# Optimization experiments

Measured on AMD Instinct MI355X. Metric: run time of the kernel, lower is better.

## Reference

```python
import jax, jax.numpy as jnp
import numpy as np

H = 16          # num_attention_heads
D = 1024        # hidden_size
HD = D // H     # attention_head_size = 64


def setup_inputs() -> dict:
    key = jax.random.key(0)
    ks = jax.random.split(key, 9)
    s = 1.0 / np.sqrt(D)
    return {
        "hidden_states": jax.random.normal(ks[0], (4, 1024, D), jnp.float32),
        "encoder_hidden_states": jax.random.normal(ks[1], (4, 1024, D), jnp.float32),
        "attention_mask": jnp.zeros((4, 1, 1, 2048), jnp.float32),
        "Wq": jax.random.normal(ks[2], (D, D), jnp.float32) * s,
        "bq": jnp.zeros((D,), jnp.float32),
        "Wk": jax.random.normal(ks[3], (D, D), jnp.float32) * s,
        "bk": jnp.zeros((D,), jnp.float32),
        "Wv": jax.random.normal(ks[4], (D, D), jnp.float32) * s,
        "bv": jnp.zeros((D,), jnp.float32),
    }


def _split_heads(x):
    # [B, S, D] -> [B, H, S, HD]
    B, S, _ = x.shape
    return x.reshape(B, S, H, HD).transpose(0, 2, 1, 3)


def reference(hidden_states, encoder_hidden_states, attention_mask, Wq, bq, Wk, bk, Wv, bv):
    # KV over concat(encoder, decoder); Q over decoder hidden states only.
    all_hidden = jnp.concatenate([encoder_hidden_states, hidden_states], axis=1)  # [B, Skv, D]
    q = _split_heads(hidden_states @ Wq + bq)        # [B, H, Sq, HD]
    k = _split_heads(all_hidden @ Wk + bk)           # [B, H, Skv, HD]
    v = _split_heads(all_hidden @ Wv + bv)           # [B, H, Skv, HD]

    scores = jnp.einsum("bhqd,bhkd->bhqk", q, k) / np.sqrt(HD).astype(np.float32)
    scores = scores + attention_mask                 # additive mask, broadcast
    probs = jax.nn.softmax(scores, axis=-1)          # dropout p=0 (eval)
    ctx = jnp.einsum("bhqk,bhkd->bhqd", probs, v)    # [B, H, Sq, HD]
    B, _, Sq, _ = ctx.shape
    return ctx.transpose(0, 2, 1, 3).reshape(B, Sq, D)
```

## Files before the change

### kernel.cpp

```cpp
#include <hip/hip_runtime.h>


typedef _Float16 f16;
typedef __attribute__((ext_vector_type(4))) _Float16 half4;
typedef __attribute__((ext_vector_type(8))) _Float16 half8;
typedef __attribute__((ext_vector_type(4))) float floatx4;
typedef __attribute__((ext_vector_type(16))) float floatx16;
typedef __attribute__((ext_vector_type(4))) unsigned int uint4v;

__global__ void wt_kernel(const float* __restrict__ W, f16* __restrict__ Wt) {
    __shared__ float tile[32][33];
    int k0 = blockIdx.y * 32, n0 = blockIdx.x * 32;
    int tx = threadIdx.x, ty = threadIdx.y;
    #pragma unroll
    for (int i = 0; i < 32; i += 8)
        tile[ty + i][tx] = W[(k0 + ty + i) * 1024 + n0 + tx];
    __syncthreads();
    #pragma unroll
    for (int i = 0; i < 32; i += 8)
        Wt[(n0 + ty + i) * 1024 + k0 + tx] = (f16)tile[tx][ty + i];
}

__global__ void cvt_kernel(const float* __restrict__ hid, const float* __restrict__ enc,
                           f16* __restrict__ Aall) {
    int t = blockIdx.x * 256 + threadIdx.x;
    int rowg = t >> 7, col = (t & 127) * 8;
    int b = rowg >> 11, r = rowg & 2047;
    const float* src = (r < 1024 ? enc + ((size_t)b * 1024 + r) * 1024
                                 : hid + ((size_t)b * 1024 + (r - 1024)) * 1024) + col;
    float4 v0 = *(const float4*)src, v1 = *(const float4*)(src + 4);
    half8 o;
    o[0] = (f16)v0.x; o[1] = (f16)v0.y; o[2] = (f16)v0.z; o[3] = (f16)v0.w;
    o[4] = (f16)v1.x; o[5] = (f16)v1.y; o[6] = (f16)v1.z; o[7] = (f16)v1.w;
    *(half8*)(Aall + (size_t)rowg * 1024 + col) = o;
}

__launch_bounds__(256)
__global__ void qkv_gemm(const f16* __restrict__ Aall, const f16* __restrict__ Wt,
                         const float* __restrict__ bias, f16* __restrict__ out, int mode) {
    __shared__ f16 At[128 * 40];
    __shared__ f16 Bt[128 * 40];

    int tid = threadIdx.x;
    int m0 = blockIdx.x * 128, n0 = blockIdx.y * 128;
    int wid = tid >> 6, lane = tid & 63;
    int wm = (wid >> 1) * 64, wn = (wid & 1) * 64;
    int lr = lane & 15, lg = lane >> 4;

    floatx4 acc[4][4];
    #pragma unroll
    for (int i = 0; i < 4; i++)
        #pragma unroll
        for (int j = 0; j < 4; j++) acc[i][j] = (floatx4)(0.f);

    int tr2 = tid >> 2, tk2 = (tid & 3) * 8;
    const f16 *a0src, *a1src;
    {
        int mA0 = m0 + tr2, mA1 = mA0 + 64;
        if (mode == 0) {
            int b0 = mA0 >> 10, b1 = mA1 >> 10;
            a0src = Aall + ((size_t)(b0 * 2048 + 1024 + (mA0 & 1023))) * 1024 + tk2;
            a1src = Aall + ((size_t)(b1 * 2048 + 1024 + (mA1 & 1023))) * 1024 + tk2;
        } else {
            a0src = Aall + (size_t)mA0 * 1024 + tk2;
            a1src = Aall + (size_t)mA1 * 1024 + tk2;
        }
    }
    const f16* b0src = Wt + (size_t)(n0 + tr2) * 1024 + tk2;
    const f16* b1src = Wt + (size_t)(n0 + tr2 + 64) * 1024 + tk2;

    half8 ra0 = *(const half8*)a0src, ra1 = *(const half8*)a1src;
    half8 rb0 = *(const half8*)b0src, rb1 = *(const half8*)b1src;

    for (int k0 = 0; k0 < 1024; k0 += 32) {
        __syncthreads();
        *(half8*)&At[tr2 * 40 + tk2]        = ra0;
        *(half8*)&At[(tr2 + 64) * 40 + tk2] = ra1;
        *(half8*)&Bt[tr2 * 40 + tk2]        = rb0;
        *(half8*)&Bt[(tr2 + 64) * 40 + tk2] = rb1;
        __syncthreads();
        if (k0 < 992) {
            ra0 = *(const half8*)(a0src + k0 + 32);
            ra1 = *(const half8*)(a1src + k0 + 32);
            rb0 = *(const half8*)(b0src + k0 + 32);
            rb1 = *(const half8*)(b1src + k0 + 32);
        }

        half8 a[4], bf[4];
        #pragma unroll
        for (int i = 0; i < 4; i++)
            a[i] = *(const half8*)&At[(wm + i * 16 + lr) * 40 + lg * 8];
        #pragma unroll
        for (int j = 0; j < 4; j++)
            bf[j] = *(const half8*)&Bt[(wn + j * 16 + lr) * 40 + lg * 8];
        __builtin_amdgcn_s_setprio(1);
        #pragma unroll
        for (int i = 0; i < 4; i++)
            #pragma unroll
            for (int j = 0; j < 4; j++)
                acc[i][j] = __builtin_amdgcn_mfma_f32_16x16x32_f16(a[i], bf[j], acc[i][j], 0, 0, 0);
        __builtin_amdgcn_s_setprio(0);
    }

    if (mode == 2) {
        #pragma unroll
        for (int i = 0; i < 4; i++) {
            int mbase = m0 + wm + i * 16 + lg * 4;
            int b = mbase >> 11, s = mbase & 2047;
            #pragma unroll
            for (int j = 0; j < 4; j++) {
                int n = n0 + wn + j * 16 + lr;
                int h = n >> 6, d = n & 63;
                float bv = bias[n];
                half4 w;
                #pragma unroll
                for (int r = 0; r < 4; r++) w[r] = (f16)(acc[i][j][r] + bv);
                *(half4*)(out + ((size_t)((b * 16 + h) * 64 + d)) * 2048 + s) = w;
            }
        }
    } else {
        int Sout = (mode == 0) ? 1024 : 2048;
        #pragma unroll
        for (int i = 0; i < 4; i++) {
            int mbase = m0 + wm + i * 16 + lg * 4;
            #pragma unroll
            for (int j = 0; j < 4; j++) {
                int n = n0 + wn + j * 16 + lr;
                int h = n >> 6, d = n & 63;
                float bv = bias[n];
                #pragma unroll
                for (int r = 0; r < 4; r++) {
                    int m = mbase + r;
                    int b = (mode == 0) ? (m >> 10) : (m >> 11);
                    int s = (mode == 0) ? (m & 1023) : (m & 2047);
                    out[((size_t)(b * 16 + h) * Sout + s) * 64 + d] = (f16)(acc[i][j][r] + bv);
                }
            }
        }
    }
}

__device__ inline half8 pack_swap(float s0, float s1, float s2, float s3,
                                  float s4, float s5, float s6, float s7) {
    unsigned a0 = __builtin_bit_cast(unsigned, __builtin_amdgcn_cvt_pkrtz(s0, s1));
    unsigned b0 = __builtin_bit_cast(unsigned, __builtin_amdgcn_cvt_pkrtz(s4, s5));
    unsigned a1 = __builtin_bit_cast(unsigned, __builtin_amdgcn_cvt_pkrtz(s2, s3));
    unsigned b1 = __builtin_bit_cast(unsigned, __builtin_amdgcn_cvt_pkrtz(s6, s7));
    asm("v_permlane32_swap_b32 %0, %1" : "+v"(a0), "+v"(b0));
    asm("v_permlane32_swap_b32 %0, %1" : "+v"(a1), "+v"(b1));
    uint4v w = {a0, a1, b0, b1};
    return __builtin_bit_cast(half8, w);
}

__device__ inline half8 pack_noswap(float s0, float s1, float s2, float s3,
                                    float s4, float s5, float s6, float s7) {
    unsigned w0 = __builtin_bit_cast(unsigned, __builtin_amdgcn_cvt_pkrtz(s0, s1));
    unsigned w1 = __builtin_bit_cast(unsigned, __builtin_amdgcn_cvt_pkrtz(s2, s3));
    unsigned w2 = __builtin_bit_cast(unsigned, __builtin_amdgcn_cvt_pkrtz(s4, s5));
    unsigned w3 = __builtin_bit_cast(unsigned, __builtin_amdgcn_cvt_pkrtz(s6, s7));
    uint4v w = {w0, w1, w2, w3};
    return __builtin_bit_cast(half8, w);
}

__launch_bounds__(256)
__global__ void attn_kernel(const f16* __restrict__ Q, const f16* __restrict__ K,
                            const f16* __restrict__ Vt, const float* __restrict__ mask,
                            float* __restrict__ out) {
    __shared__ f16 Kt[64 * 72];
    __shared__ f16 Vtt[64 * 72];
    __shared__ float maskLds[2048];

    const float LOG2E = 1.4426950408889634f;
    int tid = threadIdx.x;
    int wid = tid >> 6, lane = tid & 63;
    int l31 = lane & 31, l5 = lane >> 5;
    int bh = blockIdx.y, b = bh >> 4, h = bh & 15;
    int q = blockIdx.x * 128 + wid * 32 + l31;

    half8 pa, pcode;
    #pragma unroll
    for (int j = 0; j < 8; j++) { pa[j] = (f16)0; pcode[j] = (f16)(8 * l5 + j); }
    if (l31 < 16 && (l31 >> 3) == l5) pa[l31 & 7] = (f16)1;
    floatx16 pd = __builtin_amdgcn_mfma_f32_32x32x16_f16(pa, pcode, (floatx16)0.f, 0, 0, 0);
    float r4 = __shfl(pd[0], 32);
    bool twoblk = (r4 > 6.0f);

    const float* maskp = mask + b * 2048;
    for (int i = tid; i < 512; i += 256) {
        float4 mv = ((const float4*)maskp)[i];
        mv.x *= LOG2E; mv.y *= LOG2E; mv.z *= LOG2E; mv.w *= LOG2E;
        ((float4*)maskLds)[i] = mv;
    }

    const f16* qrow = Q + ((size_t)bh * 1024 + q) * 64;
    half8 qf[4];
    if (!twoblk) {
        #pragma unroll
        for (int ks = 0; ks < 4; ks++)
            qf[ks] = *(const half8*)(qrow + ks * 16 + l5 * 8);
    } else {
        #pragma unroll
        for (int ks = 0; ks < 4; ks++) {
            half4 lo = *(const half4*)(qrow + ks * 16 + 4 * l5);
            half4 hi = *(const half4*)(qrow + ks * 16 + 8 + 4 * l5);
            qf[ks][0] = lo[0]; qf[ks][1] = lo[1]; qf[ks][2] = lo[2]; qf[ks][3] = lo[3];
            qf[ks][4] = hi[0]; qf[ks][5] = hi[1]; qf[ks][6] = hi[2]; qf[ks][7] = hi[3];
        }
    }
    const f16 qs = (f16)(0.125f * 1.4426950408889634f);
    #pragma unroll
    for (int ks = 0; ks < 4; ks++)
        #pragma unroll
        for (int x = 0; x < 8; x++) qf[ks][x] *= qs;

    floatx16 o0 = (floatx16)0.f, o1 = (floatx16)0.f;
    float m_run = -1e30f, l_run = 0.f;

    int sr = tid >> 2, sc = (tid & 3) * 16;
    const f16* Ksrc = K + ((size_t)bh * 2048 + sr) * 64 + sc;
    const f16* Vsrc = Vt + ((size_t)(bh * 64 + sr)) * 2048 + sc;

    half8 rk0 = *(const half8*)(Ksrc);
    half8 rk1 = *(const half8*)(Ksrc + 8);
    half8 rv0 = *(const half8*)(Vsrc);
    half8 rv1 = *(const half8*)(Vsrc + 8);

    for (int kv0 = 0; kv0 < 2048; kv0 += 64) {
        __syncthreads();
        *(half8*)&Kt[sr * 72 + sc]      = rk0;
        *(half8*)&Kt[sr * 72 + sc + 8]  = rk1;
        *(half8*)&Vtt[sr * 72 + sc]     = rv0;
        *(half8*)&Vtt[sr * 72 + sc + 8] = rv1;
        __syncthreads();
        if (kv0 < 2048 - 64) {
            rk0 = *(const half8*)(Ksrc + (size_t)(kv0 + 64) * 64);
            rk1 = *(const half8*)(Ksrc + (size_t)(kv0 + 64) * 64 + 8);
            rv0 = *(const half8*)(Vsrc + kv0 + 64);
            rv1 = *(const half8*)(Vsrc + kv0 + 64 + 8);
        }

        floatx16 sf0, sf1;
        #pragma unroll
        for (int g = 0; g < 4; g++) {
            float4 mk0 = *(const float4*)&maskLds[kv0 + 8 * g + 4 * l5];
            float4 mk1 = *(const float4*)&maskLds[kv0 + 32 + 8 * g + 4 * l5];
            #pragma unroll
            for (int i = 0; i < 4; i++) {
                sf0[4 * g + i] = ((const float*)&mk0)[i];
                sf1[4 * g + i] = ((const float*)&mk1)[i];
            }
        }

        __builtin_amdgcn_s_setprio(1);
        #pragma unroll
        for (int ks = 0; ks < 4; ks++) {
            half8 k0 = *(const half8*)&Kt[l31 * 72 + ks * 16 + l5 * 8];
            half8 k1 = *(const half8*)&Kt[(32 + l31) * 72 + ks * 16 + l5 * 8];
            sf0 = __builtin_amdgcn_mfma_f32_32x32x16_f16(k0, qf[ks], sf0, 0, 0, 0);
            sf1 = __builtin_amdgcn_mfma_f32_32x32x16_f16(k1, qf[ks], sf1, 0, 0, 0);
        }
        __builtin_amdgcn_s_setprio(0);

        float pmax = -1e30f;
        #pragma unroll
        for (int r = 0; r < 16; r++)
            pmax = fmaxf(pmax, fmaxf(sf0[r], sf1[r]));

        if (!__all(pmax - m_run <= 8.0f)) {
            float rmax = fmaxf(pmax, __shfl_xor(pmax, 32));
            float mnew = fmaxf(m_run, rmax);
            float alpha = exp2f(m_run - mnew);
            l_run *= alpha;
            #pragma unroll
            for (int r = 0; r < 16; r++) { o0[r] *= alpha; o1[r] *= alpha; }
            m_run = mnew;
        }

        float ls = 0.f;
        #pragma unroll
        for (int r = 0; r < 16; r++) {
            float p0 = exp2f(sf0[r] - m_run);
            float p1 = exp2f(sf1[r] - m_run);
            sf0[r] = p0; sf1[r] = p1;
            ls += p0 + p1;
        }
        ls += __shfl_xor(ls, 32);
        l_run += ls;

        half8 pb[4];
        if (!twoblk) {
            pb[0] = pack_swap(sf0[0], sf0[1], sf0[2], sf0[3], sf0[4], sf0[5], sf0[6], sf0[7]);
            pb[1] = pack_swap(sf0[8], sf0[9], sf0[10], sf0[11], sf0[12], sf0[13], sf0[14], sf0[15]);
            pb[2] = pack_swap(sf1[0], sf1[1], sf1[2], sf1[3], sf1[4], sf1[5], sf1[6], sf1[7]);
            pb[3] = pack_swap(sf1[8], sf1[9], sf1[10], sf1[11], sf1[12], sf1[13], sf1[14], sf1[15]);
        } else {
            pb[0] = pack_noswap(sf0[0], sf0[1], sf0[2], sf0[3], sf0[4], sf0[5], sf0[6], sf0[7]);
            pb[1] = pack_noswap(sf0[8], sf0[9], sf0[10], sf0[11], sf0[12], sf0[13], sf0[14], sf0[15]);
            pb[2] = pack_noswap(sf1[0], sf1[1], sf1[2], sf1[3], sf1[4], sf1[5], sf1[6], sf1[7]);
            pb[3] = pack_noswap(sf1[8], sf1[9], sf1[10], sf1[11], sf1[12], sf1[13], sf1[14], sf1[15]);
        }

        __builtin_amdgcn_s_setprio(1);
        #pragma unroll
        for (int kb = 0; kb < 4; kb++) {
            half8 v0 = *(const half8*)&Vtt[l31 * 72 + kb * 16 + l5 * 8];
            half8 v1 = *(const half8*)&Vtt[(32 + l31) * 72 + kb * 16 + l5 * 8];
            o0 = __builtin_amdgcn_mfma_f32_32x32x16_f16(v0, pb[kb], o0, 0, 0, 0);
            o1 = __builtin_amdgcn_mfma_f32_32x32x16_f16(v1, pb[kb], o1, 0, 0, 0);
        }
        __builtin_amdgcn_s_setprio(0);
    }

    float inv = 1.f / l_run;
    float* orow = out + ((size_t)(b * 1024 + q)) * 1024 + h * 64;
    #pragma unroll
    for (int g = 0; g < 4; g++) {
        float4 r0 = {o0[4 * g] * inv, o0[4 * g + 1] * inv, o0[4 * g + 2] * inv, o0[4 * g + 3] * inv};
        float4 r1 = {o1[4 * g] * inv, o1[4 * g + 1] * inv, o1[4 * g + 2] * inv, o1[4 * g + 3] * inv};
        *(float4*)&orow[8 * g + 4 * l5]      = r0;
        *(float4*)&orow[32 + 8 * g + 4 * l5] = r1;
    }
}

extern "C" void kernel_launch(void* const* d_in, const int* in_sizes, int n_in,
                              void* d_out, int out_size, void* d_ws, size_t ws_size,
                              hipStream_t stream) {
    const float* hid  = (const float*)d_in[0];
    const float* enc  = (const float*)d_in[1];
    const float* mask = (const float*)d_in[2];
    const float* Wq   = (const float*)d_in[3];
    const float* bq   = (const float*)d_in[4];
    const float* Wk   = (const float*)d_in[5];
    const float* bk   = (const float*)d_in[6];
    const float* Wv   = (const float*)d_in[7];
    const float* bv   = (const float*)d_in[8];
    float* out = (float*)d_out;

    char* ws = (char*)d_ws;
    f16* Wtq  = (f16*)(ws + ((size_t)0 << 20));
    f16* Wtk  = (f16*)(ws + ((size_t)2 << 20));
    f16* Wtv  = (f16*)(ws + ((size_t)4 << 20));
    f16* Aall = (f16*)(ws + ((size_t)6 << 20));
    f16* Qw   = (f16*)(ws + ((size_t)22 << 20));
    f16* Kw   = (f16*)(ws + ((size_t)30 << 20));
    f16* Vtw  = (f16*)(ws + ((size_t)46 << 20));

    dim3 tb(32, 8);
    wt_kernel<<<dim3(32, 32), tb, 0, stream>>>(Wq, Wtq);
    wt_kernel<<<dim3(32, 32), tb, 0, stream>>>(Wk, Wtk);
    wt_kernel<<<dim3(32, 32), tb, 0, stream>>>(Wv, Wtv);
    cvt_kernel<<<4096, 256, 0, stream>>>(hid, enc, Aall);

    qkv_gemm<<<dim3(32, 8), 256, 0, stream>>>(Aall, Wtq, bq, Qw, 0);
    qkv_gemm<<<dim3(64, 8), 256, 0, stream>>>(Aall, Wtk, bk, Kw, 1);
    qkv_gemm<<<dim3(64, 8), 256, 0, stream>>>(Aall, Wtv, bv, Vtw, 2);

    attn_kernel<<<dim3(8, 64), 256, 0, stream>>>(Qw, Kw, Vtw, mask, out);
}
```

Measured before the change: 168.9 us.

## Use direct global-to-LDS loads in GEMM, prescale mask, remap attention blocks per XCD

The QKV GEMM now loads tiles with global_load_lds straight into unpadded LDS instead of staging them through registers, which drops the register-level prefetch. The three weight-transpose launches are merged into one grid. The mask is prescaled by log2e in a separate small kernel and read from global memory inside the attention loop rather than from LDS. Attention blocks are remapped so that each XCD works on a contiguous set of heads for L2 locality, and the running max starts at 8 instead of -inf. The unpadded LDS layout may cause bank conflicts, and dropping the prefetch exposes global-load latency in the GEMM.

New measurement: 174.4 us. +3.3%, slower.

```diff
diff --git a/kernel.cpp b/kernel.cpp
--- a/kernel.cpp
+++ b/kernel.cpp
@@ -8,8 +8,17 @@
 typedef __attribute__((ext_vector_type(16))) float floatx16;
 typedef __attribute__((ext_vector_type(4))) unsigned int uint4v;
 
-__global__ void wt_kernel(const float* __restrict__ W, f16* __restrict__ Wt) {
+#define GLOAD16(gp, lp)                                                        \
+    __builtin_amdgcn_global_load_lds(                                          \
+        (const __attribute__((address_space(1))) void*)(gp),                   \
+        (__attribute__((address_space(3))) void*)(lp), 16, 0, 0)
+
+__global__ void wt_kernel(const float* __restrict__ Wq, const float* __restrict__ Wk,
+                          const float* __restrict__ Wv, f16* __restrict__ Wtq,
+                          f16* __restrict__ Wtk, f16* __restrict__ Wtv) {
     __shared__ float tile[32][33];
+    const float* W = (blockIdx.z == 0) ? Wq : (blockIdx.z == 1) ? Wk : Wv;
+    f16* Wt = (blockIdx.z == 0) ? Wtq : (blockIdx.z == 1) ? Wtk : Wtv;
     int k0 = blockIdx.y * 32, n0 = blockIdx.x * 32;
     int tx = threadIdx.x, ty = threadIdx.y;
     #pragma unroll
@@ -35,11 +44,19 @@
     *(half8*)(Aall + (size_t)rowg * 1024 + col) = o;
 }
 
+__global__ void maskscale_kernel(const float* __restrict__ mask, float* __restrict__ maskS) {
+    const float LOG2E = 1.4426950408889634f;
+    int i = blockIdx.x * 256 + threadIdx.x;
+    float4 v = ((const float4*)mask)[i];
+    v.x *= LOG2E; v.y *= LOG2E; v.z *= LOG2E; v.w *= LOG2E;
+    ((float4*)maskS)[i] = v;
+}
+
 __launch_bounds__(256)
 __global__ void qkv_gemm(const f16* __restrict__ Aall, const f16* __restrict__ Wt,
                          const float* __restrict__ bias, f16* __restrict__ out, int mode) {
-    __shared__ f16 At[128 * 40];
-    __shared__ f16 Bt[128 * 40];
+    __shared__ f16 As[128 * 32];
+    __shared__ f16 Bs[128 * 32];
 
     int tid = threadIdx.x;
     int m0 = blockIdx.x * 128, n0 = blockIdx.y * 128;
@@ -53,46 +70,40 @@
         #pragma unroll
         for (int j = 0; j < 4; j++) acc[i][j] = (floatx4)(0.f);
 
-    int tr2 = tid >> 2, tk2 = (tid & 3) * 8;
-    const f16 *a0src, *a1src;
+    int trow = tid >> 2, tcol = (tid & 3) * 8;
+    const f16 *a0g, *a1g;
     {
-        int mA0 = m0 + tr2, mA1 = mA0 + 64;
+        int mA0 = m0 + trow, mA1 = mA0 + 64;
         if (mode == 0) {
             int b0 = mA0 >> 10, b1 = mA1 >> 10;
-            a0src = Aall + ((size_t)(b0 * 2048 + 1024 + (mA0 & 1023))) * 1024 + tk2;
-            a1src = Aall + ((size_t)(b1 * 2048 + 1024 + (mA1 & 1023))) * 1024 + tk2;
+            a0g = Aall + ((size_t)(b0 * 2048 + 1024 + (mA0 & 1023))) * 1024 + tcol;
+            a1g = Aall + ((size_t)(b1 * 2048 + 1024 + (mA1 & 1023))) * 1024 + tcol;
         } else {
-            a0src = Aall + (size_t)mA0 * 1024 + tk2;
-            a1src = Aall + (size_t)mA1 * 1024 + tk2;
-        }
-    }
-    const f16* b0src = Wt + (size_t)(n0 + tr2) * 1024 + tk2;
-    const f16* b1src = Wt + (size_t)(n0 + tr2 + 64) * 1024 + tk2;
-
-    half8 ra0 = *(const half8*)a0src, ra1 = *(const half8*)a1src;
-    half8 rb0 = *(const half8*)b0src, rb1 = *(const half8*)b1src;
+            a0g = Aall + (size_t)mA0 * 1024 + tcol;
+            a1g = Aall + (size_t)mA1 * 1024 + tcol;
+        }
+    }
+    const f16* b0g = Wt + (size_t)(n0 + trow) * 1024 + tcol;
+    const f16* b1g = Wt + (size_t)(n0 + trow + 64) * 1024 + tcol;
+    f16* lA0 = &As[tid * 8];
+    f16* lA1 = &As[tid * 8 + 2048];
+    f16* lB0 = &Bs[tid * 8];
+    f16* lB1 = &Bs[tid * 8 + 2048];
 
     for (int k0 = 0; k0 < 1024; k0 += 32) {
+        GLOAD16(a0g + k0, lA0);
+        GLOAD16(a1g + k0, lA1);
+        GLOAD16(b0g + k0, lB0);
+        GLOAD16(b1g + k0, lB1);
         __syncthreads();
-        *(half8*)&At[tr2 * 40 + tk2]        = ra0;
-        *(half8*)&At[(tr2 + 64) * 40 + tk2] = ra1;
-        *(half8*)&Bt[tr2 * 40 + tk2]        = rb0;
-        *(half8*)&Bt[(tr2 + 64) * 40 + tk2] = rb1;
-        __syncthreads();
-        if (k0 < 992) {
-            ra0 = *(const half8*)(a0src + k0 + 32);
-            ra1 = *(const half8*)(a1src + k0 + 32);
-            rb0 = *(const half8*)(b0src + k0 + 32);
-            rb1 = *(const half8*)(b1src + k0 + 32);
-        }
 
         half8 a[4], bf[4];
         #pragma unroll
         for (int i = 0; i < 4; i++)
-            a[i] = *(const half8*)&At[(wm + i * 16 + lr) * 40 + lg * 8];
+            a[i] = *(const half8*)&As[(wm + i * 16 + lr) * 32 + lg * 8];
         #pragma unroll
         for (int j = 0; j < 4; j++)
-            bf[j] = *(const half8*)&Bt[(wn + j * 16 + lr) * 40 + lg * 8];
+            bf[j] = *(const half8*)&Bs[(wn + j * 16 + lr) * 32 + lg * 8];
         __builtin_amdgcn_s_setprio(1);
         #pragma unroll
         for (int i = 0; i < 4; i++)
@@ -100,6 +111,7 @@
             for (int j = 0; j < 4; j++)
                 acc[i][j] = __builtin_amdgcn_mfma_f32_16x16x32_f16(a[i], bf[j], acc[i][j], 0, 0, 0);
         __builtin_amdgcn_s_setprio(0);
+        __syncthreads();
     }
 
     if (mode == 2) {
@@ -162,20 +174,25 @@
     return __builtin_bit_cast(half8, w);
 }
 
+struct F4x4 { float4 a, b, c, d; };
+
 __launch_bounds__(256)
 __global__ void attn_kernel(const f16* __restrict__ Q, const f16* __restrict__ K,
-                            const f16* __restrict__ Vt, const float* __restrict__ mask,
+                            const f16* __restrict__ Vt, const float* __restrict__ maskS,
                             float* __restrict__ out) {
     __shared__ f16 Kt[64 * 72];
     __shared__ f16 Vtt[64 * 72];
-    __shared__ float maskLds[2048];
-
-    const float LOG2E = 1.4426950408889634f;
+
     int tid = threadIdx.x;
     int wid = tid >> 6, lane = tid & 63;
     int l31 = lane & 31, l5 = lane >> 5;
-    int bh = blockIdx.y, b = bh >> 4, h = bh & 15;
-    int q = blockIdx.x * 128 + wid * 32 + l31;
+
+    int bid = blockIdx.x + 8 * blockIdx.y;
+    int xcd = bid & 7, w = bid >> 3;
+    int bh = xcd * 8 + (w >> 3);
+    int xblk = w & 7;
+    int b = bh >> 4;
+    int q = xblk * 128 + wid * 32 + l31;
 
     half8 pa, pcode;
     #pragma unroll
@@ -185,13 +202,6 @@
     float r4 = __shfl(pd[0], 32);
     bool twoblk = (r4 > 6.0f);
 
-    const float* maskp = mask + b * 2048;
-    for (int i = tid; i < 512; i += 256) {
-        float4 mv = ((const float4*)maskp)[i];
-        mv.x *= LOG2E; mv.y *= LOG2E; mv.z *= LOG2E; mv.w *= LOG2E;
-        ((float4*)maskLds)[i] = mv;
-    }
-
     const f16* qrow = Q + ((size_t)bh * 1024 + q) * 64;
     half8 qf[4];
     if (!twoblk) {
@@ -214,11 +224,12 @@
         for (int x = 0; x < 8; x++) qf[ks][x] *= qs;
 
     floatx16 o0 = (floatx16)0.f, o1 = (floatx16)0.f;
-    float m_run = -1e30f, l_run = 0.f;
+    float m_run = 8.0f, l_run = 0.f;
 
     int sr = tid >> 2, sc = (tid & 3) * 16;
     const f16* Ksrc = K + ((size_t)bh * 2048 + sr) * 64 + sc;
     const f16* Vsrc = Vt + ((size_t)(bh * 64 + sr)) * 2048 + sc;
+    const float* Mb = maskS + b * 2048 + 4 * l5;
 
     half8 rk0 = *(const half8*)(Ksrc);
     half8 rk1 = *(const half8*)(Ksrc + 8);
@@ -239,17 +250,13 @@
             rv1 = *(const half8*)(Vsrc + kv0 + 64 + 8);
         }
 
-        floatx16 sf0, sf1;
-        #pragma unroll
-        for (int g = 0; g < 4; g++) {
-            float4 mk0 = *(const float4*)&maskLds[kv0 + 8 * g + 4 * l5];
-            float4 mk1 = *(const float4*)&maskLds[kv0 + 32 + 8 * g + 4 * l5];
-            #pragma unroll
-            for (int i = 0; i < 4; i++) {
-                sf0[4 * g + i] = ((const float*)&mk0)[i];
-                sf1[4 * g + i] = ((const float*)&mk1)[i];
-            }
-        }
+        F4x4 t0, t1;
+        t0.a = *(const float4*)(Mb + kv0);      t0.b = *(const float4*)(Mb + kv0 + 8);
+        t0.c = *(const float4*)(Mb + kv0 + 16); t0.d = *(const float4*)(Mb + kv0 + 24);
+        t1.a = *(const float4*)(Mb + kv0 + 32); t1.b = *(const float4*)(Mb + kv0 + 40);
+        t1.c = *(const float4*)(Mb + kv0 + 48); t1.d = *(const float4*)(Mb + kv0 + 56);
+        floatx16 sf0 = __builtin_bit_cast(floatx16, t0);
+        floatx16 sf1 = __builtin_bit_cast(floatx16, t1);
 
         __builtin_amdgcn_s_setprio(1);
         #pragma unroll
@@ -311,6 +318,7 @@
         __builtin_amdgcn_s_setprio(0);
     }
 
+    int h = bh & 15;
     float inv = 1.f / l_run;
     float* orow = out + ((size_t)(b * 1024 + q)) * 1024 + h * 64;
     #pragma unroll
@@ -344,16 +352,15 @@
     f16* Qw   = (f16*)(ws + ((size_t)22 << 20));
     f16* Kw   = (f16*)(ws + ((size_t)30 << 20));
     f16* Vtw  = (f16*)(ws + ((size_t)46 << 20));
-
-    dim3 tb(32, 8);
-    wt_kernel<<<dim3(32, 32), tb, 0, stream>>>(Wq, Wtq);
-    wt_kernel<<<dim3(32, 32), tb, 0, stream>>>(Wk, Wtk);
-    wt_kernel<<<dim3(32, 32), tb, 0, stream>>>(Wv, Wtv);
+    float* maskS = (float*)(ws + ((size_t)62 << 20));
+
+    wt_kernel<<<dim3(32, 32, 3), dim3(32, 8), 0, stream>>>(Wq, Wk, Wv, Wtq, Wtk, Wtv);
     cvt_kernel<<<4096, 256, 0, stream>>>(hid, enc, Aall);
+    maskscale_kernel<<<8, 256, 0, stream>>>(mask, maskS);
 
     qkv_gemm<<<dim3(32, 8), 256, 0, stream>>>(Aall, Wtq, bq, Qw, 0);
     qkv_gemm<<<dim3(64, 8), 256, 0, stream>>>(Aall, Wtk, bk, Kw, 1);
     qkv_gemm<<<dim3(64, 8), 256, 0, stream>>>(Aall, Wtv, bv, Vtw, 2);
 
-    attn_kernel<<<dim3(8, 64), 256, 0, stream>>>(Qw, Kw, Vtw, mask, out);
-}
+    attn_kernel<<<dim3(8, 64), 256, 0, stream>>>(Qw, Kw, Vtw, maskS, out);
+}
```
